# Kernel tuning notes

Measured on AMD Instinct MI355X. Metric: run time of the kernel, lower is better.

The kernel has to match this reference:

```python
import jax, jax.numpy as jnp
import numpy as np

DIM = 512
NUM_HEADS = 8
HEAD_DIM = DIM // NUM_HEADS
SCALE = HEAD_DIM ** -0.5


def setup_inputs() -> dict:
    key = jax.random.key(0)
    ks = jax.random.split(key, 5)
    B, N = 4, 2048
    x = jax.random.normal(ks[0], (B, N, DIM), dtype=jnp.float32)
    # Learned parameters (torch nn.Linear style: y = x @ W.T + b)
    w_qkv = jax.random.normal(ks[1], (3 * DIM, DIM), dtype=jnp.float32) * (DIM ** -0.5)
    b_qkv = jnp.zeros((3 * DIM,), dtype=jnp.float32)
    w_proj = jax.random.normal(ks[2], (DIM, DIM), dtype=jnp.float32) * (DIM ** -0.5)
    b_proj = jnp.zeros((DIM,), dtype=jnp.float32)
    return {"x": x, "w_qkv": w_qkv, "b_qkv": b_qkv, "w_proj": w_proj, "b_proj": b_proj}


def reference(x, w_qkv, b_qkv, w_proj, b_proj):
    B, N, C = x.shape
    qkv = x @ w_qkv.T + b_qkv                      # [B, N, 3C]
    qkv = qkv.reshape(B, N, 3, NUM_HEADS, HEAD_DIM)
    qkv = jnp.transpose(qkv, (2, 0, 3, 1, 4))      # [3, B, H, N, d]
    q, k, v = qkv[0], qkv[1], qkv[2]
    attn = jnp.einsum("bhqd,bhkd->bhqk", q, k) * SCALE  # [B, H, N, N]
    attn = jax.nn.softmax(attn, axis=-1)
    out = jnp.einsum("bhqk,bhkd->bhqd", attn, v)   # [B, H, N, d]
    out = jnp.transpose(out, (0, 2, 1, 3)).reshape(B, N, C)
    return out @ w_proj.T + b_proj
```

## Files before the change

kernel.cpp:

```cpp
#include <hip/hip_runtime.h>

#define DIM 512
#define NHEAD 8
#define HDIM 64
#define BATCH 4
#define SEQ 2048
#define MTOT (BATCH*SEQ)
#define SCALE 0.125f
#define LOG2E 1.4426950408889634f

typedef __bf16 bf16_t;
typedef __bf16 bf16x8 __attribute__((ext_vector_type(8)));
typedef __bf16 bf16x4 __attribute__((ext_vector_type(4)));
typedef float f32x4 __attribute__((ext_vector_type(4)));

#define ASYNC_COPY16(g, l) __builtin_amdgcn_global_load_lds( \
    (const __attribute__((address_space(1))) void*)(g),      \
    (__attribute__((address_space(3))) void*)(l), 16, 0, 0)

#define NX_ELEM  (4194304)
#define NWQ_ELEM (786432)
#define NWP_ELEM (262144)
__global__ __launch_bounds__(256) void cvt_kernel(const float* __restrict__ x,
                                                  const float* __restrict__ wq,
                                                  const float* __restrict__ wp,
                                                  bf16_t* __restrict__ out) {
    int i = (blockIdx.x * 256 + threadIdx.x) * 4;
    const float* src;
    if (i < NX_ELEM)                 src = x  + i;
    else if (i < NX_ELEM + NWQ_ELEM) src = wq + (i - NX_ELEM);
    else                             src = wp + (i - NX_ELEM - NWQ_ELEM);
    float4 v = *reinterpret_cast<const float4*>(src);
    bf16x4 o;
    o[0] = (bf16_t)v.x; o[1] = (bf16_t)v.y; o[2] = (bf16_t)v.z; o[3] = (bf16_t)v.w;
    *reinterpret_cast<bf16x4*>(out + i) = o;
}

__global__ __launch_bounds__(256) void gemm_qkv_kernel(
    const bf16_t* __restrict__ X, const bf16_t* __restrict__ W,
    const float* __restrict__ bias,
    bf16_t* __restrict__ Qo, bf16_t* __restrict__ Ko, bf16_t* __restrict__ Vto)
{
    __shared__ bf16_t As[128][64];
    __shared__ bf16_t Bs[128][64];
    const int tid = threadIdx.x;
    const int wave = tid >> 6, lane = tid & 63;
    const int lhi = lane >> 4, llo = lane & 15;
    const int o = blockIdx.x;
    const int x = o & 7, i0 = o >> 3;
    const int m0 = (x * 8 + (i0 & 7)) * 128;
    const int n0 = (i0 >> 3) * 128;
    const int wr = (wave >> 1) * 64, wc = (wave & 1) * 64;
    f32x4 acc[4][4] = {};

    const int srow = wave * 32 + (lane >> 3);
    const int scol = (lane & 7) * 8;
    const bf16_t* gA = X + (size_t)(m0 + srow) * DIM + scol;
    const bf16_t* gB = W + (size_t)(n0 + srow) * DIM + scol;

    for (int k0 = 0; k0 < DIM; k0 += 64) {
        #pragma unroll
        for (int p = 0; p < 4; ++p) {
            ASYNC_COPY16(gA + (size_t)p * 8 * DIM + k0, &As[wave*32 + p*8][0]);
            ASYNC_COPY16(gB + (size_t)p * 8 * DIM + k0, &Bs[wave*32 + p*8][0]);
        }
        __syncthreads();
        #pragma unroll
        for (int ks = 0; ks < 2; ++ks) {
            bf16x8 af[4], bfr[4];
            #pragma unroll
            for (int i = 0; i < 4; ++i)
                af[i] = *reinterpret_cast<const bf16x8*>(&As[wr + i*16 + llo][ks*32 + lhi*8]);
            #pragma unroll
            for (int j = 0; j < 4; ++j)
                bfr[j] = *reinterpret_cast<const bf16x8*>(&Bs[wc + j*16 + llo][ks*32 + lhi*8]);
            __builtin_amdgcn_s_setprio(1);
            #pragma unroll
            for (int i = 0; i < 4; ++i)
                #pragma unroll
                for (int j = 0; j < 4; ++j)
                    acc[i][j] = __builtin_amdgcn_mfma_f32_16x16x32_bf16(af[i], bfr[j], acc[i][j], 0, 0, 0);
            __builtin_amdgcn_s_setprio(0);
        }
        __syncthreads();
    }

    #pragma unroll
    for (int j = 0; j < 4; ++j) {
        int col = n0 + wc + j*16 + llo;
        int which = col >> 9;
        int hh = (col >> 6) & 7;
        int dd = col & 63;
        float bv = bias[col];
        #pragma unroll
        for (int i = 0; i < 4; ++i) {
            #pragma unroll
            for (int r = 0; r < 4; ++r) {
                int m = m0 + wr + i*16 + lhi*4 + r;
                int b = m >> 11, ns = m & 2047;
                float v = acc[i][j][r] + bv;
                size_t bh = (size_t)(b * NHEAD + hh);
                if (which == 0)
                    Qo[(bh * SEQ + ns) * HDIM + dd] = (bf16_t)(v * (SCALE * LOG2E));
                else if (which == 1)
                    Ko[(bh * SEQ + ns) * HDIM + dd] = (bf16_t)v;
                else
                    Vto[(bh * HDIM + dd) * SEQ + ns] = (bf16_t)v;
            }
        }
    }
}

__global__ __launch_bounds__(512) void attn_kernel(
    const bf16_t* __restrict__ Q, const bf16_t* __restrict__ K,
    const bf16_t* __restrict__ Vt, bf16_t* __restrict__ O)
{
    __shared__ bf16_t Ks[2][64][64];
    __shared__ bf16_t Vs[2][64][64];
    const int tid = threadIdx.x;
    const int wave = tid >> 6, lane = tid & 63;
    const int lhi = lane >> 4, llo = lane & 15;
    const int o = blockIdx.x;
    const int w = (o & 7) * 32 + (o >> 3);
    const int qt = w & 7, bh = w >> 3;
    const bf16_t* Qb = Q + (size_t)bh * SEQ * HDIM;
    const bf16_t* Kb = K + (size_t)bh * SEQ * HDIM;
    const bf16_t* Vb = Vt + (size_t)bh * HDIM * SEQ;
    const int q0 = qt * 256 + wave * 32;

    const int ksr = tid >> 3, kg = tid & 7;
    const int kcol = (kg * 8) ^ ((ksr & 7) * 8);
    const int vd = tid >> 3, vg = tid & 7;
    const int pkA = (32*(vg>>2) + 8*((2*vg)&3)   + 4*((vg>>1)&1)) ^ ((vd & 7) * 8);
    const int pkB = (32*(vg>>2) + 8*((2*vg+1)&3) + 4*((vg>>1)&1)) ^ ((vd & 7) * 8);

    bf16x8 aq[2][2];
    #pragma unroll
    for (int qb = 0; qb < 2; ++qb)
        #pragma unroll
        for (int ks = 0; ks < 2; ++ks)
            aq[qb][ks] = *reinterpret_cast<const bf16x8*>(
                Qb + (size_t)(q0 + qb*16 + llo) * HDIM + ks*32 + lhi*8);

    f32x4 acc_o[2][4] = {};
    float mstat[2], lstat[2];
    mstat[0] = mstat[1] = -1e30f;
    lstat[0] = lstat[1] = 0.f;
    const float THR = 8.0f * LOG2E;

    uint4 kreg, vreg;
    kreg = *reinterpret_cast<const uint4*>(Kb + (size_t)ksr * HDIM + kg*8);
    vreg = *reinterpret_cast<const uint4*>(Vb + (size_t)vd * SEQ + vg*8);
    *reinterpret_cast<uint4*>(&Ks[0][ksr][kcol]) = kreg;
    *reinterpret_cast<uint2*>(&Vs[0][vd][pkA]) = make_uint2(vreg.x, vreg.y);
    *reinterpret_cast<uint2*>(&Vs[0][vd][pkB]) = make_uint2(vreg.z, vreg.w);
    __syncthreads();

    const int NT = SEQ / 64;
    for (int kt = 0; kt < NT; ++kt) {
        const int cur = kt & 1, nxt = cur ^ 1;

        if (kt + 1 < NT) {
            const size_t koff = (size_t)(kt + 1) * 64;
            kreg = *reinterpret_cast<const uint4*>(Kb + (koff + ksr) * HDIM + kg*8);
            vreg = *reinterpret_cast<const uint4*>(Vb + (size_t)vd * SEQ + koff + vg*8);
        }

        f32x4 s[2][4] = {};
        __builtin_amdgcn_s_setprio(1);
        #pragma unroll
        for (int kb = 0; kb < 4; ++kb) {
            #pragma unroll
            for (int ks = 0; ks < 2; ++ks) {
                bf16x8 kf = *reinterpret_cast<const bf16x8*>(
                    &Ks[cur][kb*16 + llo][(ks*32 + lhi*8) ^ ((llo & 7) * 8)]);
                #pragma unroll
                for (int qb = 0; qb < 2; ++qb)
                    s[qb][kb] = __builtin_amdgcn_mfma_f32_16x16x32_bf16(kf, aq[qb][ks], s[qb][kb], 0, 0, 0);
            }
        }
        __builtin_amdgcn_s_setprio(0);

        float lmax[2];
        bool ok = true;
        #pragma unroll
        for (int qb = 0; qb < 2; ++qb) {
            float mx = s[qb][0][0];
            #pragma unroll
            for (int kb = 0; kb < 4; ++kb)
                #pragma unroll
                for (int r = 0; r < 4; ++r) mx = fmaxf(mx, s[qb][kb][r]);
            lmax[qb] = mx;
            ok &= (mx <= mstat[qb] + THR);
        }

        if (!__all(ok)) {
            #pragma unroll
            for (int qb = 0; qb < 2; ++qb) {
                float mx = lmax[qb];
                mx = fmaxf(mx, __shfl_xor(mx, 16, 64));
                mx = fmaxf(mx, __shfl_xor(mx, 32, 64));
                float mold = mstat[qb];
                float mn = fmaxf(mold, mx);
                float alpha = __builtin_amdgcn_exp2f(mold - mn);
                mstat[qb] = mn;
                lstat[qb] *= alpha;
                #pragma unroll
                for (int r = 0; r < 4; ++r) {
                    float av = __shfl(alpha, (lane & 48) >> 2 | r, 64);
                    #pragma unroll
                    for (int db = 0; db < 4; ++db) acc_o[qb][db][r] *= av;
                }
            }
        }

        float rs[2] = {0.f, 0.f};
        #pragma unroll
        for (int kp = 0; kp < 2; ++kp) {
            bf16x8 ap[2];
            #pragma unroll
            for (int qb = 0; qb < 2; ++qb) {
                #pragma unroll
                for (int j = 0; j < 4; ++j) {
                    float p0 = __builtin_amdgcn_exp2f(s[qb][2*kp][j]     - mstat[qb]);
                    float p1 = __builtin_amdgcn_exp2f(s[qb][2*kp + 1][j] - mstat[qb]);
                    rs[qb] += p0 + p1;
                    ap[qb][j]     = (bf16_t)p0;
                    ap[qb][4 + j] = (bf16_t)p1;
                }
            }
            __builtin_amdgcn_s_setprio(1);
            #pragma unroll
            for (int db = 0; db < 4; ++db) {
                bf16x8 bv = *reinterpret_cast<const bf16x8*>(
                    &Vs[cur][db*16 + llo][(kp*32 + lhi*8) ^ ((llo & 7) * 8)]);
                #pragma unroll
                for (int qb = 0; qb < 2; ++qb)
                    acc_o[qb][db] = __builtin_amdgcn_mfma_f32_16x16x32_bf16(ap[qb], bv, acc_o[qb][db], 0, 0, 0);
            }
            __builtin_amdgcn_s_setprio(0);
        }
        #pragma unroll
        for (int qb = 0; qb < 2; ++qb) {
            float r = rs[qb];
            r += __shfl_xor(r, 16, 64);
            r += __shfl_xor(r, 32, 64);
            lstat[qb] += r;
        }

        if (kt + 1 < NT) {
            *reinterpret_cast<uint4*>(&Ks[nxt][ksr][kcol]) = kreg;
            *reinterpret_cast<uint2*>(&Vs[nxt][vd][pkA]) = make_uint2(vreg.x, vreg.y);
            *reinterpret_cast<uint2*>(&Vs[nxt][vd][pkB]) = make_uint2(vreg.z, vreg.w);
        }
        __syncthreads();
    }

    const int b = bh >> 3, h = bh & 7;
    #pragma unroll
    for (int qb = 0; qb < 2; ++qb) {
        float inv = 1.0f / lstat[qb];
        #pragma unroll
        for (int r = 0; r < 4; ++r) {
            float iv = __shfl(inv, (lane & 48) >> 2 | r, 64);
            int q = q0 + qb*16 + lhi*4 + r;
            #pragma unroll
            for (int db = 0; db < 4; ++db)
                O[(size_t)(b * SEQ + q) * DIM + h*HDIM + db*16 + llo] =
                    (bf16_t)(acc_o[qb][db][r] * iv);
        }
    }
}

__global__ __launch_bounds__(256) void gemm_proj_kernel(
    const bf16_t* __restrict__ X, const bf16_t* __restrict__ W,
    const float* __restrict__ bias, float* __restrict__ out)
{
    __shared__ bf16_t As[128][64];
    __shared__ bf16_t Bs[128][64];
    const int tid = threadIdx.x;
    const int wave = tid >> 6, lane = tid & 63;
    const int lhi = lane >> 4, llo = lane & 15;
    const int o = blockIdx.x;
    const int x = o & 7, i0 = o >> 3;
    const int m0 = (x * 8 + (i0 & 7)) * 128;
    const int n0 = (i0 >> 3) * 128;
    const int wr = (wave >> 1) * 64, wc = (wave & 1) * 64;
    f32x4 acc[4][4] = {};

    const int srow = wave * 32 + (lane >> 3);
    const int scol = (lane & 7) * 8;
    const bf16_t* gA = X + (size_t)(m0 + srow) * DIM + scol;
    const bf16_t* gB = W + (size_t)(n0 + srow) * DIM + scol;

    for (int k0 = 0; k0 < DIM; k0 += 64) {
        #pragma unroll
        for (int p = 0; p < 4; ++p) {
            ASYNC_COPY16(gA + (size_t)p * 8 * DIM + k0, &As[wave*32 + p*8][0]);
            ASYNC_COPY16(gB + (size_t)p * 8 * DIM + k0, &Bs[wave*32 + p*8][0]);
        }
        __syncthreads();
        #pragma unroll
        for (int ks = 0; ks < 2; ++ks) {
            bf16x8 af[4], bfr[4];
            #pragma unroll
            for (int i = 0; i < 4; ++i)
                af[i] = *reinterpret_cast<const bf16x8*>(&As[wr + i*16 + llo][ks*32 + lhi*8]);
            #pragma unroll
            for (int j = 0; j < 4; ++j)
                bfr[j] = *reinterpret_cast<const bf16x8*>(&Bs[wc + j*16 + llo][ks*32 + lhi*8]);
            __builtin_amdgcn_s_setprio(1);
            #pragma unroll
            for (int i = 0; i < 4; ++i)
                #pragma unroll
                for (int j = 0; j < 4; ++j)
                    acc[i][j] = __builtin_amdgcn_mfma_f32_16x16x32_bf16(af[i], bfr[j], acc[i][j], 0, 0, 0);
            __builtin_amdgcn_s_setprio(0);
        }
        __syncthreads();
    }

    #pragma unroll
    for (int j = 0; j < 4; ++j) {
        int col = n0 + wc + j*16 + llo;
        float bv = bias[col];
        #pragma unroll
        for (int i = 0; i < 4; ++i)
            #pragma unroll
            for (int r = 0; r < 4; ++r) {
                int m = m0 + wr + i*16 + lhi*4 + r;
                out[(size_t)m * DIM + col] = acc[i][j][r] + bv;
            }
    }
}

extern "C" void kernel_launch(void* const* d_in, const int* in_sizes, int n_in,
                              void* d_out, int out_size, void* d_ws, size_t ws_size,
                              hipStream_t stream) {
    const float* x      = (const float*)d_in[0];
    const float* w_qkv  = (const float*)d_in[1];
    const float* b_qkv  = (const float*)d_in[2];
    const float* w_proj = (const float*)d_in[3];
    const float* b_proj = (const float*)d_in[4];
    float* out = (float*)d_out;

    const size_t NX  = (size_t)MTOT * DIM;
    const size_t NWQ = (size_t)3 * DIM * DIM;
    const size_t NWP = (size_t)DIM * DIM;
    const size_t NQ  = (size_t)BATCH * NHEAD * SEQ * HDIM;

    bf16_t* Xb    = (bf16_t*)d_ws;
    bf16_t* Wqkv  = Xb + NX;
    bf16_t* Wproj = Wqkv + NWQ;
    bf16_t* Qb    = Wproj + NWP;
    bf16_t* Kb    = Qb + NQ;
    bf16_t* Vtb   = Kb + NQ;
    bf16_t* AOb   = Vtb + NQ;

    cvt_kernel<<<(int)((NX + NWQ + NWP) / 1024), 256, 0, stream>>>(x, w_qkv, w_proj, Xb);

    gemm_qkv_kernel<<<768, 256, 0, stream>>>(Xb, Wqkv, b_qkv, Qb, Kb, Vtb);

    attn_kernel<<<256, 512, 0, stream>>>(Qb, Kb, Vtb, AOb);

    gemm_proj_kernel<<<256, 256, 0, stream>>>(AOb, Wproj, b_proj, out);
}
```

Before: 93.64 us.

## Double-buffer GEMM LDS tiles and software-pipeline PV MFMA across attention iterations

Both GEMM kernels get double-buffered LDS so the async global-to-LDS copies for the next k-tile are issued before computing the current one, which removes one barrier per iteration. The attention kernel peels its first tile and defers each tile's P·V MFMAs to the next iteration, keeping P fragments and V fragments in registers so the exp work of one tile overlaps the matrix work of the previous one. The row-sum shuffle reduction is moved out of the loop to the end. The cost is higher register pressure and twice the LDS in the GEMMs, which may lower occupancy. The attention path also adds an extra flush of the pending MFMAs when the running max is rescaled.

```diff
diff --git a/kernel.cpp b/kernel.cpp
--- a/kernel.cpp
+++ b/kernel.cpp
@@ -41,8 +41,8 @@
     const float* __restrict__ bias,
     bf16_t* __restrict__ Qo, bf16_t* __restrict__ Ko, bf16_t* __restrict__ Vto)
 {
-    __shared__ bf16_t As[128][64];
-    __shared__ bf16_t Bs[128][64];
+    __shared__ bf16_t As[2][128][64];
+    __shared__ bf16_t Bs[2][128][64];
     const int tid = threadIdx.x;
     const int wave = tid >> 6, lane = tid & 63;
     const int lhi = lane >> 4, llo = lane & 15;
@@ -58,22 +58,32 @@
     const bf16_t* gA = X + (size_t)(m0 + srow) * DIM + scol;
     const bf16_t* gB = W + (size_t)(n0 + srow) * DIM + scol;
 
-    for (int k0 = 0; k0 < DIM; k0 += 64) {
-        #pragma unroll
-        for (int p = 0; p < 4; ++p) {
-            ASYNC_COPY16(gA + (size_t)p * 8 * DIM + k0, &As[wave*32 + p*8][0]);
-            ASYNC_COPY16(gB + (size_t)p * 8 * DIM + k0, &Bs[wave*32 + p*8][0]);
-        }
-        __syncthreads();
+    #pragma unroll
+    for (int p = 0; p < 4; ++p) {
+        ASYNC_COPY16(gA + (size_t)p * 8 * DIM, &As[0][wave*32 + p*8][0]);
+        ASYNC_COPY16(gB + (size_t)p * 8 * DIM, &Bs[0][wave*32 + p*8][0]);
+    }
+    __syncthreads();
+
+    for (int ki = 0; ki < 8; ++ki) {
+        const int cur = ki & 1, nxt = cur ^ 1;
+        if (ki + 1 < 8) {
+            const int k0n = (ki + 1) * 64;
+            #pragma unroll
+            for (int p = 0; p < 4; ++p) {
+                ASYNC_COPY16(gA + (size_t)p * 8 * DIM + k0n, &As[nxt][wave*32 + p*8][0]);
+                ASYNC_COPY16(gB + (size_t)p * 8 * DIM + k0n, &Bs[nxt][wave*32 + p*8][0]);
+            }
+        }
         #pragma unroll
         for (int ks = 0; ks < 2; ++ks) {
             bf16x8 af[4], bfr[4];
             #pragma unroll
             for (int i = 0; i < 4; ++i)
-                af[i] = *reinterpret_cast<const bf16x8*>(&As[wr + i*16 + llo][ks*32 + lhi*8]);
+                af[i] = *reinterpret_cast<const bf16x8*>(&As[cur][wr + i*16 + llo][ks*32 + lhi*8]);
             #pragma unroll
             for (int j = 0; j < 4; ++j)
-                bfr[j] = *reinterpret_cast<const bf16x8*>(&Bs[wc + j*16 + llo][ks*32 + lhi*8]);
+                bfr[j] = *reinterpret_cast<const bf16x8*>(&Bs[cur][wc + j*16 + llo][ks*32 + lhi*8]);
             __builtin_amdgcn_s_setprio(1);
             #pragma unroll
             for (int i = 0; i < 4; ++i)
@@ -144,11 +154,15 @@
 
     f32x4 acc_o[2][4] = {};
     float mstat[2], lstat[2];
-    mstat[0] = mstat[1] = -1e30f;
     lstat[0] = lstat[1] = 0.f;
     const float THR = 8.0f * LOG2E;
+    const int NT = SEQ / 64;
 
     uint4 kreg, vreg;
+
+    bf16x8 apA[2][2], apB[2][2];
+    bf16x8 bvA[2][4], bvB[2][4];
+
     kreg = *reinterpret_cast<const uint4*>(Kb + (size_t)ksr * HDIM + kg*8);
     vreg = *reinterpret_cast<const uint4*>(Vb + (size_t)vd * SEQ + vg*8);
     *reinterpret_cast<uint4*>(&Ks[0][ksr][kcol]) = kreg;
@@ -156,20 +170,70 @@
     *reinterpret_cast<uint2*>(&Vs[0][vd][pkB]) = make_uint2(vreg.z, vreg.w);
     __syncthreads();
 
-    const int NT = SEQ / 64;
-    for (int kt = 0; kt < NT; ++kt) {
+    kreg = *reinterpret_cast<const uint4*>(Kb + (size_t)(64 + ksr) * HDIM + kg*8);
+    vreg = *reinterpret_cast<const uint4*>(Vb + (size_t)vd * SEQ + 64 + vg*8);
+
+    {
+        f32x4 s[2][4] = {};
+        __builtin_amdgcn_s_setprio(1);
+        #pragma unroll
+        for (int kb = 0; kb < 4; ++kb)
+            #pragma unroll
+            for (int ks = 0; ks < 2; ++ks) {
+                bf16x8 kf = *reinterpret_cast<const bf16x8*>(
+                    &Ks[0][kb*16 + llo][(ks*32 + lhi*8) ^ ((llo & 7) * 8)]);
+                #pragma unroll
+                for (int qb = 0; qb < 2; ++qb)
+                    s[qb][kb] = __builtin_amdgcn_mfma_f32_16x16x32_bf16(kf, aq[qb][ks], s[qb][kb], 0, 0, 0);
+            }
+        __builtin_amdgcn_s_setprio(0);
+        #pragma unroll
+        for (int qb = 0; qb < 2; ++qb) {
+            float mx = s[qb][0][0];
+            #pragma unroll
+            for (int kb = 0; kb < 4; ++kb)
+                #pragma unroll
+                for (int r = 0; r < 4; ++r) mx = fmaxf(mx, s[qb][kb][r]);
+            mx = fmaxf(mx, __shfl_xor(mx, 16, 64));
+            mx = fmaxf(mx, __shfl_xor(mx, 32, 64));
+            mstat[qb] = mx;
+            float rs = 0.f;
+            #pragma unroll
+            for (int kp = 0; kp < 2; ++kp)
+                #pragma unroll
+                for (int j = 0; j < 4; ++j) {
+                    float p0 = __builtin_amdgcn_exp2f(s[qb][2*kp][j]     - mx);
+                    float p1 = __builtin_amdgcn_exp2f(s[qb][2*kp + 1][j] - mx);
+                    rs += p0 + p1;
+                    apA[qb][kp][j]     = (bf16_t)p0;
+                    apA[qb][kp][4 + j] = (bf16_t)p1;
+                }
+            lstat[qb] = rs;
+        }
+        #pragma unroll
+        for (int kp = 0; kp < 2; ++kp)
+            #pragma unroll
+            for (int db = 0; db < 4; ++db)
+                bvA[kp][db] = *reinterpret_cast<const bf16x8*>(
+                    &Vs[0][db*16 + llo][(kp*32 + lhi*8) ^ ((llo & 7) * 8)]);
+        *reinterpret_cast<uint4*>(&Ks[1][ksr][kcol]) = kreg;
+        *reinterpret_cast<uint2*>(&Vs[1][vd][pkA]) = make_uint2(vreg.x, vreg.y);
+        *reinterpret_cast<uint2*>(&Vs[1][vd][pkB]) = make_uint2(vreg.z, vreg.w);
+        __syncthreads();
+    }
+
+    auto body = [&](int kt, bf16x8 (&apIn)[2][2], bf16x8 (&bvIn)[2][4],
+                    bf16x8 (&apOut)[2][2], bf16x8 (&bvOut)[2][4]) {
         const int cur = kt & 1, nxt = cur ^ 1;
-
         if (kt + 1 < NT) {
             const size_t koff = (size_t)(kt + 1) * 64;
             kreg = *reinterpret_cast<const uint4*>(Kb + (koff + ksr) * HDIM + kg*8);
             vreg = *reinterpret_cast<const uint4*>(Vb + (size_t)vd * SEQ + koff + vg*8);
         }
-
         f32x4 s[2][4] = {};
         __builtin_amdgcn_s_setprio(1);
         #pragma unroll
-        for (int kb = 0; kb < 4; ++kb) {
+        for (int kb = 0; kb < 4; ++kb)
             #pragma unroll
             for (int ks = 0; ks < 2; ++ks) {
                 bf16x8 kf = *reinterpret_cast<const bf16x8*>(
@@ -178,7 +242,6 @@
                 for (int qb = 0; qb < 2; ++qb)
                     s[qb][kb] = __builtin_amdgcn_mfma_f32_16x16x32_bf16(kf, aq[qb][ks], s[qb][kb], 0, 0, 0);
             }
-        }
         __builtin_amdgcn_s_setprio(0);
 
         float lmax[2];
@@ -193,8 +256,20 @@
             lmax[qb] = mx;
             ok &= (mx <= mstat[qb] + THR);
         }
-
         if (!__all(ok)) {
+            #pragma unroll
+            for (int kp = 0; kp < 2; ++kp)
+                #pragma unroll
+                for (int db = 0; db < 4; ++db)
+                    #pragma unroll
+                    for (int qb = 0; qb < 2; ++qb)
+                        acc_o[qb][db] = __builtin_amdgcn_mfma_f32_16x16x32_bf16(apIn[qb][kp], bvIn[kp][db], acc_o[qb][db], 0, 0, 0);
+            #pragma unroll
+            for (int kp = 0; kp < 2; ++kp)
+                #pragma unroll
+                for (int db = 0; db < 4; ++db)
+                    #pragma unroll
+                    for (int e = 0; e < 8; ++e) bvIn[kp][db][e] = (bf16_t)0.f;
             #pragma unroll
             for (int qb = 0; qb < 2; ++qb) {
                 float mx = lmax[qb];
@@ -214,39 +289,36 @@
             }
         }
 
-        float rs[2] = {0.f, 0.f};
+        __builtin_amdgcn_s_setprio(1);
         #pragma unroll
         for (int kp = 0; kp < 2; ++kp) {
-            bf16x8 ap[2];
             #pragma unroll
             for (int qb = 0; qb < 2; ++qb) {
+                float rs = 0.f;
                 #pragma unroll
                 for (int j = 0; j < 4; ++j) {
                     float p0 = __builtin_amdgcn_exp2f(s[qb][2*kp][j]     - mstat[qb]);
                     float p1 = __builtin_amdgcn_exp2f(s[qb][2*kp + 1][j] - mstat[qb]);
-                    rs[qb] += p0 + p1;
-                    ap[qb][j]     = (bf16_t)p0;
-                    ap[qb][4 + j] = (bf16_t)p1;
+                    rs += p0 + p1;
+                    apOut[qb][kp][j]     = (bf16_t)p0;
+                    apOut[qb][kp][4 + j] = (bf16_t)p1;
                 }
-            }
-            __builtin_amdgcn_s_setprio(1);
-            #pragma unroll
-            for (int db = 0; db < 4; ++db) {
-                bf16x8 bv = *reinterpret_cast<const bf16x8*>(
+                lstat[qb] += rs;
+            }
+            #pragma unroll
+            for (int db = 0; db < 4; ++db)
+                #pragma unroll
+                for (int qb = 0; qb < 2; ++qb)
+                    acc_o[qb][db] = __builtin_amdgcn_mfma_f32_16x16x32_bf16(apIn[qb][kp], bvIn[kp][db], acc_o[qb][db], 0, 0, 0);
+        }
+        __builtin_amdgcn_s_setprio(0);
+
+        #pragma unroll
+        for (int kp = 0; kp < 2; ++kp)
+            #pragma unroll
+            for (int db = 0; db < 4; ++db)
+                bvOut[kp][db] = *reinterpret_cast<const bf16x8*>(
                     &Vs[cur][db*16 + llo][(kp*32 + lhi*8) ^ ((llo & 7) * 8)]);
-                #pragma unroll
-                for (int qb = 0; qb < 2; ++qb)
-                    acc_o[qb][db] = __builtin_amdgcn_mfma_f32_16x16x32_bf16(ap[qb], bv, acc_o[qb][db], 0, 0, 0);
-            }
-            __builtin_amdgcn_s_setprio(0);
-        }
-        #pragma unroll
-        for (int qb = 0; qb < 2; ++qb) {
-            float r = rs[qb];
-            r += __shfl_xor(r, 16, 64);
-            r += __shfl_xor(r, 32, 64);
-            lstat[qb] += r;
-        }
 
         if (kt + 1 < NT) {
             *reinterpret_cast<uint4*>(&Ks[nxt][ksr][kcol]) = kreg;
@@ -254,9 +326,30 @@
             *reinterpret_cast<uint2*>(&Vs[nxt][vd][pkB]) = make_uint2(vreg.z, vreg.w);
         }
         __syncthreads();
-    }
+    };
+
+    for (int tp = 1; tp + 1 < NT; tp += 2) {
+        body(tp,     apA, bvA, apB, bvB);
+        body(tp + 1, apB, bvB, apA, bvA);
+    }
+    body(NT - 1, apA, bvA, apB, bvB);
+
+    #pragma unroll
+    for (int kp = 0; kp < 2; ++kp)
+        #pragma unroll
+        for (int db = 0; db < 4; ++db)
+            #pragma unroll
+            for (int qb = 0; qb < 2; ++qb)
+                acc_o[qb][db] = __builtin_amdgcn_mfma_f32_16x16x32_bf16(apB[qb][kp], bvB[kp][db], acc_o[qb][db], 0, 0, 0);
 
     const int b = bh >> 3, h = bh & 7;
+    #pragma unroll
+    for (int qb = 0; qb < 2; ++qb) {
+        float r = lstat[qb];
+        r += __shfl_xor(r, 16, 64);
+        r += __shfl_xor(r, 32, 64);
+        lstat[qb] = r;
+    }
     #pragma unroll
     for (int qb = 0; qb < 2; ++qb) {
         float inv = 1.0f / lstat[qb];
@@ -276,8 +369,8 @@
     const bf16_t* __restrict__ X, const bf16_t* __restrict__ W,
     const float* __restrict__ bias, float* __restrict__ out)
 {
-    __shared__ bf16_t As[128][64];
-    __shared__ bf16_t Bs[128][64];
+    __shared__ bf16_t As[2][128][64];
+    __shared__ bf16_t Bs[2][128][64];
     const int tid = threadIdx.x;
     const int wave = tid >> 6, lane = tid & 63;
     const int lhi = lane >> 4, llo = lane & 15;
@@ -293,22 +386,32 @@
     const bf16_t* gA = X + (size_t)(m0 + srow) * DIM + scol;
     const bf16_t* gB = W + (size_t)(n0 + srow) * DIM + scol;
 
-    for (int k0 = 0; k0 < DIM; k0 += 64) {
-        #pragma unroll
-        for (int p = 0; p < 4; ++p) {
-            ASYNC_COPY16(gA + (size_t)p * 8 * DIM + k0, &As[wave*32 + p*8][0]);
-            ASYNC_COPY16(gB + (size_t)p * 8 * DIM + k0, &Bs[wave*32 + p*8][0]);
-        }
-        __syncthreads();
+    #pragma unroll
+    for (int p = 0; p < 4; ++p) {
+        ASYNC_COPY16(gA + (size_t)p * 8 * DIM, &As[0][wave*32 + p*8][0]);
+        ASYNC_COPY16(gB + (size_t)p * 8 * DIM, &Bs[0][wave*32 + p*8][0]);
+    }
+    __syncthreads();
+
+    for (int ki = 0; ki < 8; ++ki) {
+        const int cur = ki & 1, nxt = cur ^ 1;
+        if (ki + 1 < 8) {
+            const int k0n = (ki + 1) * 64;
+            #pragma unroll
+            for (int p = 0; p < 4; ++p) {
+                ASYNC_COPY16(gA + (size_t)p * 8 * DIM + k0n, &As[nxt][wave*32 + p*8][0]);
+                ASYNC_COPY16(gB + (size_t)p * 8 * DIM + k0n, &Bs[nxt][wave*32 + p*8][0]);
+            }
+        }
         #pragma unroll
         for (int ks = 0; ks < 2; ++ks) {
             bf16x8 af[4], bfr[4];
             #pragma unroll
             for (int i = 0; i < 4; ++i)
-                af[i] = *reinterpret_cast<const bf16x8*>(&As[wr + i*16 + llo][ks*32 + lhi*8]);
+                af[i] = *reinterpret_cast<const bf16x8*>(&As[cur][wr + i*16 + llo][ks*32 + lhi*8]);
             #pragma unroll
             for (int j = 0; j < 4; ++j)
-                bfr[j] = *reinterpret_cast<const bf16x8*>(&Bs[wc + j*16 + llo][ks*32 + lhi*8]);
+                bfr[j] = *reinterpret_cast<const bf16x8*>(&Bs[cur][wc + j*16 + llo][ks*32 + lhi*8]);
             __builtin_amdgcn_s_setprio(1);
             #pragma unroll
             for (int i = 0; i < 4; ++i)
```

Result: no change. 95.45 us (+1.9%).
